# Kernel tuning notes

Hardware: AMD Instinct MI355X
Metric: run time of the kernel (lower is better)

Reference implementation:

```python
import jax, jax.numpy as jnp
import numpy as np

N = 20000   # nodes per graph batch
E = 160000  # edges
G = 128     # graphs in batch
F = 114     # node feature dim (num_features == num_features_xd)
H = 10      # GAT heads
HF = F * H  # 1140


def setup_inputs() -> dict:
    key = jax.random.key(0)
    ks = jax.random.split(key, 64)
    ki = iter(range(64))
    def rn(shape, scale=0.05):
        return jax.random.normal(ks[next(ki)], shape, dtype=jnp.float32) * scale
    inp = {}
    inp["x1"] = jax.random.normal(ks[next(ki)], (N, F), dtype=jnp.float32)
    inp["edge_index1"] = jax.random.randint(ks[next(ki)], (2, E), 0, N)
    inp["batch1"] = jnp.sort(jax.random.randint(ks[next(ki)], (N,), 0, G))
    inp["x2"] = jax.random.normal(ks[next(ki)], (N, F), dtype=jnp.float32)
    inp["edge_index2"] = jax.random.randint(ks[next(ki)], (2, E), 0, N)
    inp["batch2"] = jnp.sort(jax.random.randint(ks[next(ki)], (N,), 0, G))
    inp["target"] = jax.random.normal(ks[next(ki)], (G, 1000), dtype=jnp.float32)
    for p in ("p1", "p2"):
        inp[p + "_gatW"] = rn((F, HF))
        inp[p + "_att_src"] = rn((H, F))
        inp[p + "_att_dst"] = rn((H, F))
        inp[p + "_gatb"] = rn((HF,))
        inp[p + "_gcnW"] = rn((HF, HF))
        inp[p + "_gcnb"] = rn((HF,))
        inp[p + "_fcg1W"] = rn((2 * HF, 1000))
        inp[p + "_fcg1b"] = rn((1000,))
        inp[p + "_fcg2W"] = rn((1000, 64))
        inp[p + "_fcg2b"] = rn((64,))
    inp["fcxtW"] = rn((1000, 128)); inp["fcxtb"] = rn((128,))
    inp["fc1W"] = rn((256, 128)); inp["fc1b"] = rn((128,))
    inp["fc2W"] = rn((128, 32)); inp["fc2b"] = rn((32,))
    inp["outW"] = rn((32, 1)); inp["outb"] = rn((1,))
    return inp


def lrelu(v):
    return jax.nn.leaky_relu(v, 0.01)  # nn.LeakyReLU default slope


def gat_conv(x, src, dst, W, att_src, att_dst, b):
    # PyG GATConv (concat heads, add_self_loops handled by caller)
    h = (x @ W).reshape(N, H, F)                     # [N,H,F]
    a_s = jnp.sum(h * att_src[None], axis=-1)        # [N,H]
    a_d = jnp.sum(h * att_dst[None], axis=-1)        # [N,H]
    e = jax.nn.leaky_relu(a_s[src] + a_d[dst], 0.2)  # [E',H]
    m = jax.ops.segment_max(e, dst, num_segments=N)
    ex = jnp.exp(e - m[dst])
    den = jax.ops.segment_sum(ex, dst, num_segments=N)
    alpha = ex / den[dst]                            # softmax over incoming edges
    out = jax.ops.segment_sum(alpha[:, :, None] * h[src], dst, num_segments=N)
    return out.reshape(N, HF) + b


def gcn_conv(x, src, dst, W, b):
    # PyG GCNConv with self loops (added by caller), symmetric normalization
    deg = jax.ops.segment_sum(jnp.ones_like(dst, dtype=x.dtype), dst, num_segments=N)
    dinv = jax.lax.rsqrt(jnp.maximum(deg, 1.0))
    h = x @ W                                        # [N,HF]
    msg = (dinv[src] * dinv[dst])[:, None] * h[src]
    return jax.ops.segment_sum(msg, dst, num_segments=N) + b


def branch(x, edge_index, batch, gatW, a_s, a_d, gatb, gcnW, gcnb, f1W, f1b, f2W, f2b):
    loop = jnp.arange(N, dtype=edge_index.dtype)
    src = jnp.concatenate([edge_index[0], loop])
    dst = jnp.concatenate([edge_index[1], loop])
    h = lrelu(gat_conv(x, src, dst, gatW, a_s, a_d, gatb))
    h = lrelu(gcn_conv(h, src, dst, gcnW, gcnb))
    mx = jax.ops.segment_max(h, batch, num_segments=G)
    mx = jnp.where(jnp.isfinite(mx), mx, 0.0)        # guard empty graphs
    cnt = jax.ops.segment_sum(jnp.ones((N,), h.dtype), batch, num_segments=G)
    mean = jax.ops.segment_sum(h, batch, num_segments=G) / jnp.maximum(cnt, 1.0)[:, None]
    g = jnp.concatenate([mx, mean], axis=1)          # [G, 2*HF]
    g = lrelu(g @ f1W + f1b)                         # dropout is identity at eval
    return g @ f2W + f2b                             # [G, 64]


def reference(x1, edge_index1, batch1, x2, edge_index2, batch2, target,
              p1_gatW, p1_att_src, p1_att_dst, p1_gatb, p1_gcnW, p1_gcnb,
              p1_fcg1W, p1_fcg1b, p1_fcg2W, p1_fcg2b,
              p2_gatW, p2_att_src, p2_att_dst, p2_gatb, p2_gcnW, p2_gcnb,
              p2_fcg1W, p2_fcg1b, p2_fcg2W, p2_fcg2b,
              fcxtW, fcxtb, fc1W, fc1b, fc2W, fc2b, outW, outb):
    g1 = branch(x1, edge_index1, batch1, p1_gatW, p1_att_src, p1_att_dst, p1_gatb,
                p1_gcnW, p1_gcnb, p1_fcg1W, p1_fcg1b, p1_fcg2W, p1_fcg2b)
    g2 = branch(x2, edge_index2, batch2, p2_gatW, p2_att_src, p2_att_dst, p2_gatb,
                p2_gcnW, p2_gcnb, p2_fcg1W, p2_fcg1b, p2_fcg2W, p2_fcg2b)
    xd = jnp.concatenate([g1, g2], axis=1)           # [G,128]
    xt = target.reshape(-1, 1000) @ fcxtW + fcxtb    # [G,128]
    xc = jnp.concatenate([xd, xt], axis=1)           # [G,256]
    xc = lrelu(xc @ fc1W + fc1b)
    xc = lrelu(xc @ fc2W + fc2b)
    return xc @ outW + outb                          # [G,1]
```

## Files before the change

kernel.cpp:

```cpp
#include <hip/hip_runtime.h>
#include <cstddef>
#include <cstdint>

#define NN 20000
#define EE 160000
#define EPRIME 180000
#define GG 128
#define FF 114
#define HH 10
#define HFD 1140
#define KP 1152
#define F1K 2280
#define F1KS 18
#define F1KC 128
#define NSCB 79

typedef unsigned short ushort_t;
typedef __attribute__((ext_vector_type(8))) short bf16x8;
typedef __attribute__((ext_vector_type(4))) float f32x4;

static constexpr size_t REL  = (size_t)NN * KP;
static constexpr size_t ZREL = (size_t)10 * NN * 128;

static inline int cdiv(int a, int b) { return (a + b - 1) / b; }


__device__ __forceinline__ ushort_t f2bf(float v) {
    union { float f; unsigned u; } c; c.f = v;
    unsigned u = c.u;
    unsigned r = (u + 0x7fffu + ((u >> 16) & 1u)) >> 16;
    return (ushort_t)r;
}
__device__ __forceinline__ float bf2f(ushort_t h) {
    union { unsigned u; float f; } c; c.u = ((unsigned)h) << 16;
    return c.f;
}

__device__ __forceinline__ void gload16(const void* g, const ushort_t* l) {
    __builtin_amdgcn_global_load_lds(
        (const __attribute__((address_space(1))) unsigned int*)g,
        (__attribute__((address_space(3))) unsigned int*)l, 16, 0, 0);
}


__global__ void k_init(int* __restrict__ deg, int* __restrict__ gstart, int* __restrict__ gend) {
    int br = blockIdx.y;
    int i = blockIdx.x * blockDim.x + threadIdx.x;
    if (i < NN) deg[br * NN + i] = 1;
    if (i < GG) { gstart[br * GG + i] = NN; gend[br * GG + i] = 0; }
}

__global__ void k_count(const int* __restrict__ ei0, const int* __restrict__ ei1,
                        int* __restrict__ deg) {
    int br = blockIdx.y;
    const int* ei = br ? ei1 : ei0;
    int i = blockIdx.x * blockDim.x + threadIdx.x;
    if (i < EE) atomicAdd(&deg[br * NN + ei[EE + i]], 1);
}

__global__ void k_scan1(const int* __restrict__ deg, int* __restrict__ offs, int* __restrict__ bsum) {
    __shared__ int tmp[256];
    int br = blockIdx.y;
    deg += br * NN; offs += br * (NN + 1); bsum += br * 128;
    int b = blockIdx.x, tid = threadIdx.x;
    int i = b * 256 + tid;
    int v = (i < NN) ? deg[i] : 0;
    tmp[tid] = v;
    __syncthreads();
#pragma unroll
    for (int off = 1; off < 256; off <<= 1) {
        int t = (tid >= off) ? tmp[tid - off] : 0;
        __syncthreads();
        tmp[tid] += t;
        __syncthreads();
    }
    if (i < NN) offs[i + 1] = tmp[tid];
    if (tid == 255) bsum[b] = tmp[255];
}

__global__ void k_scan2(int* __restrict__ bsum) {
    __shared__ int tmp[128];
    bsum += blockIdx.y * 128;
    int tid = threadIdx.x;
    int v = (tid < NSCB) ? bsum[tid] : 0;
    tmp[tid] = v;
    __syncthreads();
#pragma unroll
    for (int off = 1; off < 128; off <<= 1) {
        int t = (tid >= off) ? tmp[tid - off] : 0;
        __syncthreads();
        tmp[tid] += t;
        __syncthreads();
    }
    if (tid < NSCB) bsum[tid] = tmp[tid] - v;
}

__global__ void k_scan3prep(int* __restrict__ offs, const int* __restrict__ bsum,
                            int* __restrict__ cursor, const int* __restrict__ deg,
                            float* __restrict__ dinv,
                            const int* __restrict__ batch0, const int* __restrict__ batch1,
                            int* __restrict__ gstart, int* __restrict__ gend) {
    int br = blockIdx.y;
    offs += br * (NN + 1); bsum += br * 128; cursor += br * NN;
    deg += br * NN; dinv += br * NN;
    const int* batch = br ? batch1 : batch0;
    gstart += br * GG; gend += br * GG;
    int i = blockIdx.x * 256 + threadIdx.x;
    if (i < NN) {
        int o = offs[i + 1] + bsum[i >> 8];
        offs[i + 1] = o;
        cursor[i] = o - deg[i];
        dinv[i] = rsqrtf((float)deg[i]);
        int b = batch[i];
        atomicMin(&gstart[b], i);
        atomicMax(&gend[b], i + 1);
    }
    if (i == 0) offs[0] = 0;
}

__global__ void k_fill(const int* __restrict__ ei0, const int* __restrict__ ei1,
                       int* __restrict__ cursor, int* __restrict__ csr) {
    int br = blockIdx.y;
    const int* ei = br ? ei1 : ei0;
    cursor += br * NN; csr += (size_t)br * EPRIME;
    int i = blockIdx.x * blockDim.x + threadIdx.x;
    if (i < EPRIME) {
        int s, d;
        if (i < EE) { s = ei[i]; d = ei[EE + i]; }
        else        { s = i - EE; d = s; }
        int pos = atomicAdd(&cursor[d], 1);
        csr[pos] = s;
    }
}


__global__ void k_split_x(const float* __restrict__ x0, const float* __restrict__ x1,
                          ushort_t* __restrict__ xb) {
    int br = blockIdx.y;
    const float* x = br ? x1 : x0;
    xb += (size_t)br * REL;
    int idx = blockIdx.x * 256 + threadIdx.x;
    if (idx >= NN * 128) return;
    int n = idx >> 7, k = idx & 127;
    float v = (k < FF) ? x[(size_t)n * FF + k] : 0.f;
    xb[idx] = f2bf(v);
}

__global__ __launch_bounds__(256) void k_tbf(const float* __restrict__ W0, const float* __restrict__ W1,
                                             int K, int Nc, int Kpad, ushort_t* __restrict__ T) {
    __shared__ float tile[64][65];
    int br = blockIdx.z;
    const float* W = br ? W1 : W0;
    T += (size_t)br * KP * KP;
    int kb = blockIdx.x * 64;
    int nb = blockIdx.y * 64;
    int c = threadIdx.x & 63, r4 = threadIdx.x >> 6;
#pragma unroll
    for (int rr = 0; rr < 16; ++rr) {
        int r = r4 * 16 + rr;
        int gk = kb + r, gn = nb + c;
        tile[r][c] = (gk < K && gn < Nc) ? W[(size_t)gk * Nc + gn] : 0.f;
    }
    __syncthreads();
#pragma unroll
    for (int rr = 0; rr < 16; ++rr) {
        int r = r4 * 16 + rr;
        int gn = nb + r, gk = kb + c;
        T[(size_t)gn * Kpad + gk] = f2bf(tile[c][r]);
    }
}

__global__ __launch_bounds__(256) void k_wgtT(const float* __restrict__ W0, const float* __restrict__ W1,
                                              ushort_t* __restrict__ WgT) {
    __shared__ float tile[64][65];
    int y = blockIdx.z;
    int br = y / 10, h = y - 10 * br;
    const float* W = br ? W1 : W0;
    ushort_t* T = WgT + ((size_t)br * 10 + h) * 128 * 128;
    int kb = blockIdx.x * 64, cb = blockIdx.y * 64;
    int c = threadIdx.x & 63, r4 = threadIdx.x >> 6;
#pragma unroll
    for (int rr = 0; rr < 16; ++rr) {
        int r = r4 * 16 + rr;
        int gk = kb + r, gc = cb + c;
        tile[r][c] = (gk < FF && gc < FF) ? W[(size_t)gk * HFD + h * FF + gc] : 0.f;
    }
    __syncthreads();
#pragma unroll
    for (int rr = 0; rr < 16; ++rr) {
        int r = r4 * 16 + rr;
        int gc2 = cb + r, gk2 = kb + c;
        T[(size_t)gc2 * 128 + gk2] = f2bf(tile[c][r]);
    }
}

__global__ void k_vsd(const float* __restrict__ W0, const float* __restrict__ W1,
                      const float* __restrict__ as0, const float* __restrict__ as1,
                      const float* __restrict__ ad0, const float* __restrict__ ad1,
                      float* __restrict__ Vs, float* __restrict__ Vd) {
    int br = blockIdx.y;
    const float* W = br ? W1 : W0;
    const float* asrc = br ? as1 : as0;
    const float* adst = br ? ad1 : ad0;
    int idx = blockIdx.x * 256 + threadIdx.x;
    if (idx >= 1280) return;
    int k = idx / 10, h = idx - 10 * (idx / 10);
    float vs = 0.f, vd = 0.f;
    if (k < FF) {
        const float* wrow = W + (size_t)k * HFD + h * FF;
        const float* s = asrc + h * FF;
        const float* d = adst + h * FF;
        for (int f = 0; f < FF; ++f) { vs += wrow[f] * s[f]; vd += wrow[f] * d[f]; }
    }
    Vs[br * 1280 + idx] = vs;
    Vd[br * 1280 + idx] = vd;
}

__global__ void k_att2(const ushort_t* __restrict__ xbase,
                       const float* __restrict__ Vs, const float* __restrict__ Vd,
                       float* __restrict__ as_, float* __restrict__ ad_) {
    int br = blockIdx.y;
    const ushort_t* xb = xbase + (size_t)br * REL;
    const float* vs = Vs + br * 1280;
    const float* vd = Vd + br * 1280;
    as_ += (size_t)br * NN * HH; ad_ += (size_t)br * NN * HH;
    int id = blockIdx.x * blockDim.x + threadIdx.x;
    if (id >= NN * HH) return;
    int n = id / HH, h = id - HH * (id / HH);
    const ushort_t* row = xb + (size_t)n * 128;
    float as = 0.f, ad = 0.f;
    for (int k = 0; k < FF; k += 2) {
        unsigned qq = *(const unsigned*)(row + k);
        float v0 = bf2f((ushort_t)(qq & 0xffffu));
        float v1 = bf2f((ushort_t)(qq >> 16));
        as += v0 * vs[k * 10 + h] + v1 * vs[(k + 1) * 10 + h];
        ad += v0 * vd[k * 10 + h] + v1 * vd[(k + 1) * 10 + h];
    }
    as_[id] = as;
    ad_[id] = ad;
}


template <int NU>
__device__ __forceinline__ void gax_grp(
    int eg, int end, int lane, float my_ad,
    const int* __restrict__ csr, const float* __restrict__ as_,
    const ushort_t* __restrict__ xb,
    float& den, float acc[HH][2]) {
    int s[NU]; float ex[NU];
#pragma unroll
    for (int u = 0; u < NU; ++u) {
        int idx = eg + u; if (idx > end - 1) idx = end - 1;
        s[u] = csr[idx];
    }
#pragma unroll
    for (int u = 0; u < NU; ++u) {
        float e = 0.f;
        if (lane < HH) {
            float t = as_[s[u] * HH + lane] + my_ad;
            t = (t >= 0.f) ? t : 0.2f * t;
            e = __expf(t);
            if (eg + u >= end) e = 0.f;
        }
        ex[u] = e;
        den += e;
    }
    unsigned xv[NU];
#pragma unroll
    for (int u = 0; u < NU; ++u)
        xv[u] = *(const unsigned*)(xb + (size_t)s[u] * 128 + 2 * lane);
#pragma unroll
    for (int u = 0; u < NU; ++u) {
        float x0 = bf2f((ushort_t)(xv[u] & 0xffffu));
        float x1 = bf2f((ushort_t)(xv[u] >> 16));
#pragma unroll
        for (int h = 0; h < HH; ++h) {
            float w = __shfl(ex[u], h, 64);
            acc[h][0] += w * x0;
            acc[h][1] += w * x1;
        }
    }
}

__global__ __launch_bounds__(256) void gat_aggx(
    const ushort_t* __restrict__ xbase,
    const float* __restrict__ as_, const float* __restrict__ ad_,
    const int* __restrict__ offs, const int* __restrict__ csr,
    ushort_t* __restrict__ Z) {
    int br = blockIdx.y;
    const ushort_t* xb = xbase + (size_t)br * REL;
    as_ += (size_t)br * NN * HH; ad_ += (size_t)br * NN * HH;
    offs += br * (NN + 1); csr += (size_t)br * EPRIME;
    ushort_t* Zb = Z + (size_t)br * ZREL;

    int lane = threadIdx.x & 63;
    int n = blockIdx.x * 4 + (threadIdx.x >> 6);
    if (n >= NN) return;
    int beg = offs[n], end = offs[n + 1];
    float my_ad = (lane < HH) ? ad_[n * HH + lane] : 0.f;

    float den = 0.f;
    float acc[HH][2];
#pragma unroll
    for (int h = 0; h < HH; ++h) { acc[h][0] = 0.f; acc[h][1] = 0.f; }

    int eg = beg;
    for (; eg + 8 <= end; eg += 8)
        gax_grp<8>(eg, end, lane, my_ad, csr, as_, xb, den, acc);
    for (; eg < end; eg += 4)
        gax_grp<4>(eg, end, lane, my_ad, csr, as_, xb, den, acc);

#pragma unroll
    for (int h = 0; h < HH; ++h) {
        float d = __shfl(den, h, 64);
        float inv = 1.f / d;
        unsigned pk = (unsigned)f2bf(acc[h][0] * inv)
                    | ((unsigned)f2bf(acc[h][1] * inv) << 16);
        *(unsigned*)(Zb + ((size_t)h * NN + n) * 128 + 2 * lane) = pk;
    }
}


__global__ __launch_bounds__(256) void mfma_hgemm(
    const ushort_t* __restrict__ Zbase, const ushort_t* __restrict__ WgT,
    const float* __restrict__ b0, const float* __restrict__ b1,
    ushort_t* __restrict__ Cbase) {
    __shared__ __align__(16) ushort_t lds[2 * 8192];
    int y = blockIdx.y;
    int br = y / 10, h = y - 10 * br;
    const ushort_t* A = Zbase + (size_t)br * ZREL + (size_t)h * NN * 128;
    const ushort_t* Bt = WgT + ((size_t)br * 10 + h) * 128 * 128;
    const float* bias = (br ? b1 : b0) + h * FF;
    ushort_t* Cb = Cbase + (size_t)br * REL;

    const int tid = threadIdx.x;
    const int lane = tid & 63;
    const int w = tid >> 6;
    const int wr = w >> 1, wc = w & 1;

    int nwg = gridDim.x;
    int q = nwg >> 3, r8 = nwg & 7;
    int xcd = blockIdx.x & 7, sidx = blockIdx.x >> 3;
    int wg = (xcd < r8 ? xcd * (q + 1) : r8 * (q + 1) + (xcd - r8) * q) + sidx;

    int row0 = wg * 128; if (row0 > NN - 128) row0 = NN - 128;

    f32x4 acc[4][4];
#pragma unroll
    for (int i = 0; i < 4; ++i)
#pragma unroll
        for (int j = 0; j < 4; ++j) acc[i][j] = (f32x4){0.f, 0.f, 0.f, 0.f};

    const char* pA[2]; const char* pB[2];
    unsigned ldsoff[2];
#pragma unroll
    for (int i = 0; i < 2; ++i) {
        int c = (w * 2 + i) * 64 + lane;
        int kg = c >> 7, r = c & 127;
        pA[i] = (const char*)A + (size_t)(row0 + r) * 256 + kg * 16;
        pB[i] = (const char*)Bt + (size_t)r * 256 + kg * 16;
        ldsoff[i] = (w * 2 + i) * 512;
    }
    const int kgf = lane >> 4, r15 = lane & 15;

    auto STAGE = [&](int buf, int ks) {
        size_t kb = (size_t)ks * 64;
        unsigned bo = buf ? 8192u : 0u;
#pragma unroll
        for (int i = 0; i < 2; ++i) {
            gload16(pA[i] + kb, lds + bo + 0 + ldsoff[i]);
            gload16(pB[i] + kb, lds + bo + 4096 + ldsoff[i]);
        }
    };

    STAGE(0, 0);
    asm volatile("s_waitcnt vmcnt(0)" ::: "memory");
    __syncthreads();
    int cur = 0;

    for (int ks = 0; ks < 4; ++ks) {
        if (ks + 1 < 4) STAGE(cur ^ 1, ks + 1);
        const ushort_t* lb = lds + (cur ? 8192u : 0u);
        bf16x8 ah[4], bh[4];
#pragma unroll
        for (int i = 0; i < 4; ++i) {
            int ra = wr * 64 + i * 16 + r15;
            int rb = wc * 64 + i * 16 + r15;
            ah[i] = *(const bf16x8*)(lb + 0 + kgf * 1024 + ra * 8);
            bh[i] = *(const bf16x8*)(lb + 4096 + kgf * 1024 + rb * 8);
        }
#pragma unroll
        for (int i = 0; i < 4; ++i)
#pragma unroll
            for (int j = 0; j < 4; ++j)
                acc[i][j] = __builtin_amdgcn_mfma_f32_16x16x32_bf16(ah[i], bh[j], acc[i][j], 0, 0, 0);
        asm volatile("s_waitcnt vmcnt(0)" ::: "memory");
        __syncthreads();
        cur ^= 1;
    }

    const int g4 = lane >> 4;
#pragma unroll
    for (int i = 0; i < 4; ++i)
#pragma unroll
        for (int j = 0; j < 4; ++j) {
            int c = wc * 64 + j * 16 + r15;
#pragma unroll
            for (int reg = 0; reg < 4; ++reg) {
                int r = row0 + wr * 64 + i * 16 + g4 * 4 + reg;
                int gc = h * FF + c;
                if (c < FF) {
                    float v = acc[i][j][reg] + bias[c];
                    v = (v >= 0.f) ? v : 0.01f * v;
                    Cb[(size_t)r * KP + gc] = f2bf(v);
                } else if (h == 9 && gc < KP) {
                    Cb[(size_t)r * KP + gc] = 0;
                }
            }
        }
}


__global__ __launch_bounds__(256) void mfma_gemm(
    const ushort_t* __restrict__ Abase, const ushort_t* __restrict__ Btbase,
    int lda, int ldb, int M, int Nreal, int ksteps, int ncb,
    ushort_t* __restrict__ Cbase, int ldcs) {
    __shared__ __align__(16) ushort_t lds[3 * 8192];
    const int br = blockIdx.y;
    const ushort_t* A = Abase + (size_t)br * REL;
    const ushort_t* Bt = Btbase + (size_t)br * KP * KP;
    ushort_t* Cb = Cbase + (size_t)br * ZREL;

    const int tid = threadIdx.x;
    const int lane = tid & 63;
    const int w = tid >> 6;
    const int wr = w >> 1, wc = w & 1;

    int nwg = gridDim.x;
    int q = nwg >> 3, r8 = nwg & 7;
    int xcd = blockIdx.x & 7, sidx = blockIdx.x >> 3;
    int wg = (xcd < r8 ? xcd * (q + 1) : r8 * (q + 1) + (xcd - r8) * q) + sidx;
    int brow = wg / ncb, bcol = wg - brow * ncb;

    int row0 = brow * 128; if (row0 > M - 128) row0 = M - 128;
    const int col0 = bcol * 128;

    f32x4 acc[4][4];
#pragma unroll
    for (int i = 0; i < 4; ++i)
#pragma unroll
        for (int j = 0; j < 4; ++j) acc[i][j] = (f32x4){0.f, 0.f, 0.f, 0.f};

    const size_t ldaB = (size_t)lda * 2, ldbB = (size_t)ldb * 2;
    const char* pA[2]; const char* pB[2];
    unsigned ldsoff[2];
#pragma unroll
    for (int i = 0; i < 2; ++i) {
        int c = (w * 2 + i) * 64 + lane;
        int kg = c >> 7, r = c & 127;
        pA[i] = (const char*)A + (size_t)(row0 + r) * ldaB + kg * 16;
        pB[i] = (const char*)Bt + (size_t)(col0 + r) * ldbB + kg * 16;
        ldsoff[i] = (w * 2 + i) * 512;
    }
    const int kgf = lane >> 4, r15 = lane & 15;

    auto STAGE = [&](int stg, int ks) {
        size_t kb = (size_t)ks * 64;
        unsigned bo = (unsigned)stg * 8192u;
#pragma unroll
        for (int i = 0; i < 2; ++i) {
            gload16(pA[i] + kb, lds + bo + 0 + ldsoff[i]);
            gload16(pB[i] + kb, lds + bo + 4096 + ldsoff[i]);
        }
    };

    STAGE(0, 0);
    STAGE(1, 1);
    asm volatile("s_waitcnt vmcnt(4)" ::: "memory");
    __builtin_amdgcn_s_barrier();
    __builtin_amdgcn_sched_barrier(0);

    for (int ks = 0; ks < ksteps; ++ks) {
        if (ks + 2 < ksteps) STAGE((ks + 2) % 3, ks + 2);
        const ushort_t* lb = lds + (ks % 3) * 8192;
        bf16x8 ah[4], bh[4];
#pragma unroll
        for (int i = 0; i < 4; ++i) {
            int ra = wr * 64 + i * 16 + r15;
            int rb = wc * 64 + i * 16 + r15;
            ah[i] = *(const bf16x8*)(lb + 0 + kgf * 1024 + ra * 8);
            bh[i] = *(const bf16x8*)(lb + 4096 + kgf * 1024 + rb * 8);
        }
#pragma unroll
        for (int i = 0; i < 4; ++i)
#pragma unroll
            for (int j = 0; j < 4; ++j)
                acc[i][j] = __builtin_amdgcn_mfma_f32_16x16x32_bf16(ah[i], bh[j], acc[i][j], 0, 0, 0);
        if (ks + 2 < ksteps) { asm volatile("s_waitcnt vmcnt(4)" ::: "memory"); }
        else                 { asm volatile("s_waitcnt vmcnt(0)" ::: "memory"); }
        __builtin_amdgcn_s_barrier();
        __builtin_amdgcn_sched_barrier(0);
    }

    const int g4 = lane >> 4;
#pragma unroll
    for (int i = 0; i < 4; ++i)
#pragma unroll
        for (int j = 0; j < 4; ++j) {
            int c = col0 + wc * 64 + j * 16 + r15;
#pragma unroll
            for (int reg = 0; reg < 4; ++reg) {
                int r = row0 + wr * 64 + i * 16 + g4 * 4 + reg;
                if (r < M) {
                    float v = (c < Nreal) ? acc[i][j][reg] : 0.f;
                    Cb[(size_t)r * ldcs + c] = f2bf(v);
                }
            }
        }
}


template <int NU>
__device__ __forceinline__ void gcn_grp(
    int eg, int end, bool act, float di,
    const int* __restrict__ csr, const float* __restrict__ dinv,
    const ushort_t* __restrict__ h2b, int kb, float* acc) {
    int s[NU]; float w[NU];
#pragma unroll
    for (int u = 0; u < NU; ++u) {
        int idx = eg + u; if (idx > end - 1) idx = end - 1;
        s[u] = csr[idx];
    }
#pragma unroll
    for (int u = 0; u < NU; ++u) {
        float ww = dinv[s[u]] * di;
        w[u] = (eg + u < end) ? ww : 0.f;
    }
    if (act) {
        bf16x8 qv[NU];
#pragma unroll
        for (int u = 0; u < NU; ++u) qv[u] = *(const bf16x8*)(h2b + (size_t)s[u] * KP + kb);
#pragma unroll
        for (int u = 0; u < NU; ++u)
#pragma unroll
            for (int e = 0; e < 8; ++e) acc[e] += w[u] * bf2f((ushort_t)qv[u][e]);
    }
}

__global__ __launch_bounds__(256) void gcn_agg(
    const ushort_t* __restrict__ h2base, const int* __restrict__ offs, const int* __restrict__ csr,
    const float* __restrict__ dinv,
    const float* __restrict__ b0, const float* __restrict__ b1,
    ushort_t* __restrict__ outbase) {
    int br = blockIdx.y;
    const ushort_t* h2b = h2base + (size_t)br * ZREL;
    offs += br * (NN + 1); csr += (size_t)br * EPRIME; dinv += br * NN;
    const float* bias = br ? b1 : b0;
    ushort_t* outb = outbase + (size_t)br * REL;

    int lane = threadIdx.x & 63;
    int qw = threadIdx.x >> 6;
    int n = blockIdx.x;
    int g = qw * 36 + lane;
    bool act = lane < 36;
    const int kb = g * 8;
    int beg = offs[n], end = offs[n + 1];
    float di = dinv[n];
    float acc[8] = {};

    int eg = beg;
    for (; eg + 8 <= end; eg += 8)
        gcn_grp<8>(eg, end, act, di, csr, dinv, h2b, kb, acc);
    for (; eg < end; eg += 4)
        gcn_grp<4>(eg, end, act, di, csr, dinv, h2b, kb, acc);

    if (act) {
        bf16x8 vb;
#pragma unroll
        for (int e = 0; e < 8; ++e) {
            int k = kb + e;
            float v = 0.f;
            if (k < HFD) {
                v = acc[e] + bias[k];
                v = (v >= 0.f) ? v : 0.01f * v;
            }
            vb[e] = (short)f2bf(v);
        }
        *(bf16x8*)(outb + (size_t)n * KP + kb) = vb;
    }
}


__global__ void k_pool(const ushort_t* __restrict__ hbase, const int* __restrict__ gs,
                       const int* __restrict__ ge, float* __restrict__ gpool) {
    int br = blockIdx.z;
    const ushort_t* hfeat = hbase + (size_t)br * REL;
    gs += br * GG; ge += br * GG;
    float* gout = gpool + (size_t)br * GG * 2 * HFD;
    if (threadIdx.x >= 48) return;
    int g = blockIdx.x;
    int mg = blockIdx.y * 48 + threadIdx.x;
    int s = gs[g], e = ge[g];
    int cnt = e - s;
    float mx[8], sm[8];
#pragma unroll
    for (int j = 0; j < 8; ++j) { mx[j] = -1e30f; sm[j] = 0.f; }
    for (int r = s; r < e; ++r) {
        bf16x8 qv = *(const bf16x8*)(hfeat + (size_t)r * KP + 8 * mg);
#pragma unroll
        for (int j = 0; j < 8; ++j) {
            float v = bf2f((ushort_t)qv[j]);
            mx[j] = fmaxf(mx[j], v);
            sm[j] += v;
        }
    }
    float inv = (cnt > 0) ? 1.f / (float)cnt : 0.f;
#pragma unroll
    for (int j = 0; j < 8; ++j) {
        int k = 8 * mg + j;
        if (k < HFD) {
            float m = (cnt > 0) ? mx[j] : 0.f;
            gout[(size_t)g * (2 * HFD) + k] = m;
            gout[(size_t)g * (2 * HFD) + HFD + k] = sm[j] * inv;
        }
    }
}


__global__ __launch_bounds__(256) void k_fcg1_part(
    const float* __restrict__ gpool, const float* __restrict__ B0, const float* __restrict__ B1,
    float* __restrict__ p0, float* __restrict__ p1) {
    __shared__ float As[16][64 + 4];
    __shared__ float Bs[16][64 + 4];
    int br = blockIdx.y >> 1, rowblk = blockIdx.y & 1;
    const float* A = gpool + (size_t)br * GG * F1K;
    const float* B = br ? B1 : B0;
    float* part = br ? p1 : p0;
    int tid = threadIdx.x;
    int tx = tid & 15, ty = tid >> 4;
    int row0 = rowblk * 64, col0 = blockIdx.x * 64;
    int kbeg = blockIdx.z * F1KC;
    float acc[4][4] = {};
#pragma unroll 1
    for (int kt = 0; kt < F1KC / 16; ++kt) {
        int kk = kbeg + kt * 16;
#pragma unroll
        for (int l = 0; l < 4; ++l) {
            int idx = tid + 256 * l;
            int m = idx >> 4, k = idx & 15;
            int gr = row0 + m, gk = kk + k;
            As[k][m] = (gk < F1K) ? A[(size_t)gr * F1K + gk] : 0.f;
        }
#pragma unroll
        for (int l = 0; l < 4; ++l) {
            int idx = tid + 256 * l;
            int nn = idx & 63, k = idx >> 6;
            int gc = col0 + nn, gk = kk + k;
            Bs[k][nn] = (gc < 1000 && gk < F1K) ? B[(size_t)gk * 1000 + gc] : 0.f;
        }
        __syncthreads();
#pragma unroll
        for (int k = 0; k < 16; ++k) {
            float4 av = *(const float4*)&As[k][ty * 4];
            float4 bv = *(const float4*)&Bs[k][tx * 4];
            float a[4] = {av.x, av.y, av.z, av.w};
            float b[4] = {bv.x, bv.y, bv.z, bv.w};
#pragma unroll
            for (int i = 0; i < 4; ++i)
#pragma unroll
                for (int j = 0; j < 4; ++j) acc[i][j] += a[i] * b[j];
        }
        __syncthreads();
    }
    float* pc = part + (size_t)blockIdx.z * GG * 1000;
#pragma unroll
    for (int i = 0; i < 4; ++i) {
        int r = row0 + ty * 4 + i;
#pragma unroll
        for (int j = 0; j < 4; ++j) {
            int c = col0 + tx * 4 + j;
            if (c < 1000) pc[(size_t)r * 1000 + c] = acc[i][j];
        }
    }
}

__global__ void k_fcg1_red(const float* __restrict__ p0, const float* __restrict__ p1,
                           const float* __restrict__ b0, const float* __restrict__ b1,
                           float* __restrict__ fc1out) {
    int br = blockIdx.y;
    const float* part = br ? p1 : p0;
    const float* bias = br ? b1 : b0;
    float* out = fc1out + (size_t)br * GG * 1000;
    int idx = blockIdx.x * 256 + threadIdx.x;
    if (idx >= GG * 1000) return;
    float s = 0.f;
#pragma unroll
    for (int k = 0; k < F1KS; ++k) s += part[(size_t)k * GG * 1000 + idx];
    int n = idx % 1000;
    float v = s + bias[n];
    out[idx] = (v >= 0.f) ? v : 0.01f * v;
}


__global__ __launch_bounds__(256) void k_fcg2(const float* __restrict__ fc1out,
                                              const float* __restrict__ W0, const float* __restrict__ W1,
                                              const float* __restrict__ b0, const float* __restrict__ b1,
                                              float* __restrict__ bout) {
    __shared__ float part[4][64];
    int br = blockIdx.y;
    const float* in = fc1out + (size_t)br * GG * 1000;
    const float* W = br ? W1 : W0;
    const float* b = br ? b1 : b0;
    float* out = bout + (size_t)br * GG * 64;
    int g = blockIdx.x;
    int o = threadIdx.x & 63, p = threadIdx.x >> 6;
    const float* row = in + (size_t)g * 1000;
    float acc = 0.f;
    for (int k = p * 250; k < (p + 1) * 250; ++k) acc += row[k] * W[k * 64 + o];
    part[p][o] = acc;
    __syncthreads();
    if (p == 0) out[(size_t)g * 64 + o] = part[0][o] + part[1][o] + part[2][o] + part[3][o] + b[o];
}


__global__ __launch_bounds__(256) void k_final(
    const float* __restrict__ b1, const float* __restrict__ b2, const float* __restrict__ target,
    const float* __restrict__ fcxtW, const float* __restrict__ fcxtb,
    const float* __restrict__ fc1W, const float* __restrict__ fc1b,
    const float* __restrict__ fc2W, const float* __restrict__ fc2b,
    const float* __restrict__ outW, const float* __restrict__ outb,
    float* __restrict__ out) {
    __shared__ float xc[256];
    __shared__ float xt2[128];
    __shared__ float y1[128];
    __shared__ float y2[32];
    int g = blockIdx.x, t = threadIdx.x;
    if (t < 64) xc[t] = b1[(size_t)g * 64 + t];
    else if (t < 128) xc[t] = b2[(size_t)g * 64 + (t - 64)];
    {
        int c = t & 127, p = t >> 7;
        float acc = 0.f;
        const float* trow = target + (size_t)g * 1000;
        for (int k = p * 500; k < (p + 1) * 500; ++k) acc += trow[k] * fcxtW[k * 128 + c];
        if (p == 1) xt2[c] = acc;
        __syncthreads();
        if (p == 0) xc[128 + c] = acc + xt2[c] + fcxtb[c];
    }
    __syncthreads();
    if (t < 128) {
        float acc = 0.f;
        for (int k = 0; k < 256; ++k) acc += xc[k] * fc1W[k * 128 + t];
        acc += fc1b[t];
        y1[t] = (acc >= 0.f) ? acc : 0.01f * acc;
    }
    __syncthreads();
    if (t < 32) {
        float acc = 0.f;
        for (int k = 0; k < 128; ++k) acc += y1[k] * fc2W[k * 32 + t];
        acc += fc2b[t];
        y2[t] = (acc >= 0.f) ? acc : 0.01f * acc;
    }
    __syncthreads();
    if (t == 0) {
        float acc = 0.f;
        for (int k = 0; k < 32; ++k) acc += y2[k] * outW[k];
        out[g] = acc + outb[0];
    }
}


extern "C" void kernel_launch(void* const* d_in, const int* in_sizes, int n_in,
                              void* d_out, int out_size, void* d_ws, size_t ws_size,
                              hipStream_t stream) {
    (void)in_sizes; (void)n_in; (void)out_size; (void)ws_size;

    size_t off = 0;
    auto alloc = [&](size_t bytes) -> void* {
        void* p = (char*)d_ws + off;
        off += (bytes + 255) & ~(size_t)255;
        return p;
    };
    char* brA = (char*)alloc(2 * ZREL * 2);
    char* brB = (char*)alloc(2 * REL * 2);
    ushort_t* Bt  = (ushort_t*)alloc(2 * (size_t)KP * KP * 2);
    ushort_t* WgT = (ushort_t*)alloc(20 * (size_t)128 * 128 * 2);
    float* Vs     = (float*)alloc(2 * 1280 * 4);
    float* Vd     = (float*)alloc(2 * 1280 * 4);
    float* a_s    = (float*)alloc(2 * (size_t)NN * HH * 4);
    float* a_d    = (float*)alloc(2 * (size_t)NN * HH * 4);
    int*   deg    = (int*)alloc(2 * (size_t)NN * 4);
    int*   offs   = (int*)alloc(2 * (size_t)(NN + 1) * 4);
    int*   cursor = (int*)alloc(2 * (size_t)NN * 4);
    int*   csr    = (int*)alloc(2 * (size_t)EPRIME * 4);
    float* dinv   = (float*)alloc(2 * (size_t)NN * 4);
    int*   gstart = (int*)alloc(2 * (size_t)GG * 4);
    int*   gend   = (int*)alloc(2 * (size_t)GG * 4);
    int*   bsum   = (int*)alloc(2 * (size_t)128 * 4);
    float* gpool  = (float*)alloc(2 * (size_t)GG * 2 * HFD * 4);
    float* fc1out = (float*)alloc(2 * (size_t)GG * 1000 * 4);
    float* bout   = (float*)alloc(2 * (size_t)GG * 64 * 4);

    ushort_t* Zb  = (ushort_t*)brA;
    float* f1p0 = (float*)brA;
    float* f1p1 = (float*)(brA + (size_t)F1KS * GG * 1000 * 4);
    ushort_t* xb  = (ushort_t*)brB;

    const float* target = (const float*)d_in[6];
    const int NRB = cdiv(NN, 128);
    const int NCB = KP / 128;

    const float* x0 = (const float*)d_in[0];
    const float* x1 = (const float*)d_in[3];
    const int* ei0 = (const int*)d_in[1];
    const int* ei1 = (const int*)d_in[4];
    const int* batch0 = (const int*)d_in[2];
    const int* batch1 = (const int*)d_in[5];
    const float *gatW0 = (const float*)d_in[7],  *gatW1 = (const float*)d_in[17];
    const float *asrc0 = (const float*)d_in[8],  *asrc1 = (const float*)d_in[18];
    const float *adst0 = (const float*)d_in[9],  *adst1 = (const float*)d_in[19];
    const float *gatb0 = (const float*)d_in[10], *gatb1 = (const float*)d_in[20];
    const float *gcnW0 = (const float*)d_in[11], *gcnW1 = (const float*)d_in[21];
    const float *gcnb0 = (const float*)d_in[12], *gcnb1 = (const float*)d_in[22];
    const float *f1W0  = (const float*)d_in[13], *f1W1  = (const float*)d_in[23];
    const float *f1b0  = (const float*)d_in[14], *f1b1  = (const float*)d_in[24];
    const float *f2W0  = (const float*)d_in[15], *f2W1  = (const float*)d_in[25];
    const float *f2b0  = (const float*)d_in[16], *f2b1  = (const float*)d_in[26];

    hipLaunchKernelGGL(k_init, dim3(cdiv(NN, 256), 2), dim3(256), 0, stream, deg, gstart, gend);
    hipLaunchKernelGGL(k_count, dim3(cdiv(EE, 256), 2), dim3(256), 0, stream, ei0, ei1, deg);
    hipLaunchKernelGGL(k_scan1, dim3(NSCB, 2), dim3(256), 0, stream, deg, offs, bsum);
    hipLaunchKernelGGL(k_scan2, dim3(1, 2), dim3(128), 0, stream, bsum);
    hipLaunchKernelGGL(k_scan3prep, dim3(NSCB, 2), dim3(256), 0, stream,
                       offs, bsum, cursor, deg, dinv, batch0, batch1, gstart, gend);
    hipLaunchKernelGGL(k_fill, dim3(cdiv(EPRIME, 256), 2), dim3(256), 0, stream, ei0, ei1, cursor, csr);

    hipLaunchKernelGGL(k_split_x, dim3(cdiv(NN * 128, 256), 2), dim3(256), 0, stream, x0, x1, xb);
    hipLaunchKernelGGL(k_wgtT, dim3(2, 2, 20), dim3(256), 0, stream, gatW0, gatW1, WgT);
    hipLaunchKernelGGL(k_vsd, dim3(5, 2), dim3(256), 0, stream,
                       gatW0, gatW1, asrc0, asrc1, adst0, adst1, Vs, Vd);

    hipLaunchKernelGGL(k_att2, dim3(cdiv(NN * HH, 256), 2), dim3(256), 0, stream,
                       xb, Vs, Vd, a_s, a_d);

    hipLaunchKernelGGL(gat_aggx, dim3(cdiv(NN, 4), 2), dim3(256), 0, stream,
                       xb, a_s, a_d, offs, csr, Zb);

    hipLaunchKernelGGL(mfma_hgemm, dim3(NRB, 20), dim3(256), 0, stream,
                       Zb, WgT, gatb0, gatb1, xb);

    hipLaunchKernelGGL(k_tbf, dim3(KP / 64, KP / 64, 2), dim3(256), 0, stream,
                       gcnW0, gcnW1, HFD, HFD, KP, Bt);

    hipLaunchKernelGGL(mfma_gemm, dim3(NRB * NCB, 2), dim3(256), 0, stream,
                       xb, Bt, KP, KP, NN, HFD, KP / 32, NCB, Zb, KP);

    hipLaunchKernelGGL(gcn_agg, dim3(NN, 2), dim3(256), 0, stream,
                       Zb, offs, csr, dinv, gcnb0, gcnb1, xb);

    hipLaunchKernelGGL(k_pool, dim3(GG, 3, 2), dim3(64), 0, stream, xb, gstart, gend, gpool);

    hipLaunchKernelGGL(k_fcg1_part, dim3(16, 4, F1KS), dim3(256), 0, stream,
                       gpool, f1W0, f1W1, f1p0, f1p1);
    hipLaunchKernelGGL(k_fcg1_red, dim3(cdiv(GG * 1000, 256), 2), dim3(256), 0, stream,
                       f1p0, f1p1, f1b0, f1b1, fc1out);

    hipLaunchKernelGGL(k_fcg2, dim3(GG, 2), dim3(256), 0, stream,
                       fc1out, f2W0, f2W1, f2b0, f2b1, bout);

    hipLaunchKernelGGL(k_final, dim3(GG), dim3(256), 0, stream,
                       bout, bout + (size_t)GG * 64, target,
                       (const float*)d_in[27], (const float*)d_in[28],
                       (const float*)d_in[29], (const float*)d_in[30],
                       (const float*)d_in[31], (const float*)d_in[32],
                       (const float*)d_in[33], (const float*)d_in[34],
                       (float*)d_out);
}
```

Baseline: 854.9 us.

## Split GCN aggregation into column tiles with one wavefront per node

The GCN neighbor aggregation used to give each node a 256-thread block in which only 36 of 64 lanes per wave were active, each loading 16-byte row chunks. It now assigns one wavefront per node and one of 9 column tiles of 128 features, with each lane handling two bf16 values through 4-byte loads. This removes the idle lanes and gives more, smaller work items. The cost is that the CSR indices and degree weights are re-read once per tile (9x) and each load is narrower.

```diff
diff --git a/kernel.cpp b/kernel.cpp
--- a/kernel.cpp
+++ b/kernel.cpp
@@ -522,9 +522,10 @@
 
 template <int NU>
 __device__ __forceinline__ void gcn_grp(
-    int eg, int end, bool act, float di,
+    int eg, int end, float di,
     const int* __restrict__ csr, const float* __restrict__ dinv,
-    const ushort_t* __restrict__ h2b, int kb, float* acc) {
+    const ushort_t* __restrict__ h2s,
+    float& a0, float& a1) {
     int s[NU]; float w[NU];
 #pragma unroll
     for (int u = 0; u < NU; ++u) {
@@ -536,14 +537,14 @@
         float ww = dinv[s[u]] * di;
         w[u] = (eg + u < end) ? ww : 0.f;
     }
-    if (act) {
-        bf16x8 qv[NU];
-#pragma unroll
-        for (int u = 0; u < NU; ++u) qv[u] = *(const bf16x8*)(h2b + (size_t)s[u] * KP + kb);
-#pragma unroll
-        for (int u = 0; u < NU; ++u)
-#pragma unroll
-            for (int e = 0; e < 8; ++e) acc[e] += w[u] * bf2f((ushort_t)qv[u][e]);
+    unsigned qv[NU];
+#pragma unroll
+    for (int u = 0; u < NU; ++u)
+        qv[u] = *(const unsigned*)(h2s + (size_t)s[u] * KP);
+#pragma unroll
+    for (int u = 0; u < NU; ++u) {
+        a0 += w[u] * bf2f((ushort_t)(qv[u] & 0xffffu));
+        a1 += w[u] * bf2f((ushort_t)(qv[u] >> 16));
     }
 }
 
@@ -552,42 +553,31 @@
     const float* __restrict__ dinv,
     const float* __restrict__ b0, const float* __restrict__ b1,
     ushort_t* __restrict__ outbase) {
-    int br = blockIdx.y;
+    int br = blockIdx.z;
+    int tile = blockIdx.y;
     const ushort_t* h2b = h2base + (size_t)br * ZREL;
     offs += br * (NN + 1); csr += (size_t)br * EPRIME; dinv += br * NN;
     const float* bias = br ? b1 : b0;
     ushort_t* outb = outbase + (size_t)br * REL;
 
     int lane = threadIdx.x & 63;
-    int qw = threadIdx.x >> 6;
-    int n = blockIdx.x;
-    int g = qw * 36 + lane;
-    bool act = lane < 36;
-    const int kb = g * 8;
+    int n = blockIdx.x * 4 + (threadIdx.x >> 6);
+    if (n >= NN) return;
+    const int k0 = tile * 128 + 2 * lane;
+    const ushort_t* h2s = h2b + k0;
     int beg = offs[n], end = offs[n + 1];
     float di = dinv[n];
-    float acc[8] = {};
+    float a0 = 0.f, a1 = 0.f;
 
     int eg = beg;
-    for (; eg + 8 <= end; eg += 8)
-        gcn_grp<8>(eg, end, act, di, csr, dinv, h2b, kb, acc);
-    for (; eg < end; eg += 4)
-        gcn_grp<4>(eg, end, act, di, csr, dinv, h2b, kb, acc);
-
-    if (act) {
-        bf16x8 vb;
-#pragma unroll
-        for (int e = 0; e < 8; ++e) {
-            int k = kb + e;
-            float v = 0.f;
-            if (k < HFD) {
-                v = acc[e] + bias[k];
-                v = (v >= 0.f) ? v : 0.01f * v;
-            }
-            vb[e] = (short)f2bf(v);
-        }
-        *(bf16x8*)(outb + (size_t)n * KP + kb) = vb;
-    }
+    for (; eg + 8 <= end; eg += 8) gcn_grp<8>(eg, end, di, csr, dinv, h2s, a0, a1);
+    for (; eg < end; eg += 4)      gcn_grp<4>(eg, end, di, csr, dinv, h2s, a0, a1);
+
+    float v0 = 0.f, v1 = 0.f;
+    if (k0 < HFD)     { v0 = a0 + bias[k0];     v0 = (v0 >= 0.f) ? v0 : 0.01f * v0; }
+    if (k0 + 1 < HFD) { v1 = a1 + bias[k0 + 1]; v1 = (v1 >= 0.f) ? v1 : 0.01f * v1; }
+    unsigned pk = (unsigned)f2bf(v0) | ((unsigned)f2bf(v1) << 16);
+    *(unsigned*)(outb + (size_t)n * KP + k0) = pk;
 }
 
 
@@ -854,7 +844,7 @@
     hipLaunchKernelGGL(mfma_gemm, dim3(NRB * NCB, 2), dim3(256), 0, stream,
                        xb, Bt, KP, KP, NN, HFD, KP / 32, NCB, Zb, KP);
 
-    hipLaunchKernelGGL(gcn_agg, dim3(NN, 2), dim3(256), 0, stream,
+    hipLaunchKernelGGL(gcn_agg, dim3(cdiv(NN, 4), 9, 2), dim3(256), 0, stream,
                        Zb, offs, csr, dinv, gcnb0, gcnb1, xb);
 
     hipLaunchKernelGGL(k_pool, dim3(GG, 3, 2), dim3(64), 0, stream, xb, gstart, gend, gpool);
```

Result: faster. 832.6 us (median of 2 runs) (-2.6%).
